# Kernel optimization log

Measured on AMD Instinct MI355X. Metric: run time of the kernel, lower is better.

## Reference

```python
import jax, jax.numpy as jnp
from jax import lax
import numpy as np

K = 3  # kernel_size

def _hamming2d():
    return jnp.asarray(np.outer(np.hamming(K), np.hamming(K)), dtype=jnp.float32)

def setup_inputs() -> dict:
    key = jax.random.key(0)
    k1, k2, k3 = jax.random.split(key, 3)
    B, C, H, W = 4, 256, 256, 256
    comp = 64
    x = jax.random.normal(k1, (B, C, H, W), dtype=jnp.float32)
    # xavier_normal for 1x1 compressor: std = sqrt(2/(fan_in+fan_out))
    w_comp = jax.random.normal(k2, (comp, C), dtype=jnp.float32) * np.sqrt(2.0 / (C + comp))
    # kernel generator: normal std=0.001, zero bias (as in _init_weights)
    w_gen = jax.random.normal(k3, (K * K, comp, 3, 3), dtype=jnp.float32) * 0.001
    b_gen = jnp.zeros((K * K,), dtype=jnp.float32)
    return {"x": x, "w_comp": w_comp, "w_gen": w_gen, "b_gen": b_gen}

def reference(x, w_comp, w_gen, b_gen):
    B, C, H, W = x.shape
    KK = K * K
    # 1x1 channel compression (no bias)
    compressed = jnp.einsum('bchw,oc->bohw', x, w_comp)
    # 3x3 conv, padding=1, with bias -> raw kernel logits (B, KK, H, W)
    logits = lax.conv_general_dilated(
        compressed, w_gen, window_strides=(1, 1), padding='SAME',
        dimension_numbers=('NCHW', 'OIHW', 'NCHW')) + b_gen[None, :, None, None]
    # softmax over the KK kernel taps per spatial position
    kw = jax.nn.softmax(logits, axis=1)
    # NOTE: original uses .view (memory reinterpret), not permute: (B,KK,H,W) -> (B,H,W,K,K)
    kw = kw.reshape(B, H, W, K, K) * _hamming2d()
    kw = kw / (kw.sum(axis=(-1, -2), keepdims=True) + 1e-8)
    kw = jnp.transpose(kw, (0, 3, 4, 1, 2)).reshape(B, KK, H, W)
    # adaptive aggregation: reflect pad + per-tap weighted sum (avoids KK x blowup)
    pad = K // 2
    xp = jnp.pad(x, ((0, 0), (0, 0), (pad, pad), (pad, pad)), mode='reflect')
    agg = jnp.zeros_like(x)
    for i in range(K):
        for j in range(K):
            agg = agg + xp[:, :, i:i + H, j:j + W] * kw[:, i * K + j][:, None]
    highpass = x - agg
    return x + highpass  # use_residual=True
```

## Files before the change

### kernel.cpp

```cpp
#include <hip/hip_runtime.h>
#include <stdint.h>

#define Bd 4
#define Cd 256
#define Hd 256
#define Wd 256
#define HW 65536
#define CM 64
#define KK 9
#define CG 32


typedef __attribute__((ext_vector_type(8))) short bf16x8;
typedef __attribute__((ext_vector_type(4))) float f32x4;

__device__ __forceinline__ uint32_t f2bf1(float f) {
    uint32_t u = __float_as_uint(f);
    return (u + 0x7FFFu + ((u >> 16) & 1u)) >> 16;
}
__device__ __forceinline__ uint32_t pkbf(float lo, float hi) {
    return f2bf1(lo) | (f2bf1(hi) << 16);
}
__device__ __forceinline__ float bf2f(uint32_t u) {
    return __uint_as_float(u << 16);
}

union BF8 { uint32_t u[4]; bf16x8 v; };

__device__ __forceinline__ void loadB(const float* __restrict__ px, int ks,
                                      float4 (&buf)[8]) {
#pragma unroll
    for (int j = 0; j < 8; ++j)
        buf[j] = *(const float4*)(px + (size_t)(ks * 32 + j) * HW);
}

__device__ __forceinline__ void stepMFMA(const float4 (&buf)[8],
                                         const short (*ws)[256], int ks,
                                         int l15, int lhi, int l7,
                                         f32x4 (&acc)[4][4]) {
    BF8 bn[4];
    bn[0].u[0] = pkbf(buf[0].x, buf[1].x);
    bn[0].u[1] = pkbf(buf[2].x, buf[3].x);
    bn[0].u[2] = pkbf(buf[4].x, buf[5].x);
    bn[0].u[3] = pkbf(buf[6].x, buf[7].x);
    bn[1].u[0] = pkbf(buf[0].y, buf[1].y);
    bn[1].u[1] = pkbf(buf[2].y, buf[3].y);
    bn[1].u[2] = pkbf(buf[4].y, buf[5].y);
    bn[1].u[3] = pkbf(buf[6].y, buf[7].y);
    bn[2].u[0] = pkbf(buf[0].z, buf[1].z);
    bn[2].u[1] = pkbf(buf[2].z, buf[3].z);
    bn[2].u[2] = pkbf(buf[4].z, buf[5].z);
    bn[2].u[3] = pkbf(buf[6].z, buf[7].z);
    bn[3].u[0] = pkbf(buf[0].w, buf[1].w);
    bn[3].u[1] = pkbf(buf[2].w, buf[3].w);
    bn[3].u[2] = pkbf(buf[4].w, buf[5].w);
    bn[3].u[3] = pkbf(buf[6].w, buf[7].w);
#pragma unroll
    for (int m = 0; m < 4; ++m) {
        int gg = ((ks << 2) + lhi) ^ l7;
        bf16x8 af = *(const bf16x8*)&ws[m * 16 + l15][gg << 3];
        acc[m][0] = __builtin_amdgcn_mfma_f32_16x16x32_bf16(af, bn[0].v, acc[m][0], 0, 0, 0);
        acc[m][1] = __builtin_amdgcn_mfma_f32_16x16x32_bf16(af, bn[1].v, acc[m][1], 0, 0, 0);
        acc[m][2] = __builtin_amdgcn_mfma_f32_16x16x32_bf16(af, bn[2].v, acc[m][2], 0, 0, 0);
        acc[m][3] = __builtin_amdgcn_mfma_f32_16x16x32_bf16(af, bn[3].v, acc[m][3], 0, 0, 0);
    }
}

__global__ __launch_bounds__(256, 2) void compress_kernel(
    const float* __restrict__ x, const float* __restrict__ w_comp,
    unsigned short* __restrict__ comp)
{
    __shared__ short ws[CM][256];

    int tid = threadIdx.x;
    {
        int o  = tid >> 2;
        int k0 = (tid & 3) << 6;
        const float* wr = w_comp + o * Cd + k0;
        int xr = o & 7;
#pragma unroll
        for (int gi = 0; gi < 8; ++gi) {
            float4 a = *(const float4*)(wr + gi * 8);
            float4 c = *(const float4*)(wr + gi * 8 + 4);
            BF8 g;
            g.u[0] = pkbf(a.x, a.y); g.u[1] = pkbf(a.z, a.w);
            g.u[2] = pkbf(c.x, c.y); g.u[3] = pkbf(c.z, c.w);
            int gg = ((k0 >> 3) + gi) ^ xr;
            *(bf16x8*)&ws[o][gg << 3] = g.v;
        }
    }
    __syncthreads();

    int lane = tid & 63;
    int wv   = tid >> 6;
    int blk  = blockIdx.x;
    int b    = blk >> 8;
    int s0   = ((blk & 255) << 8) + (wv << 6);
    int l15  = lane & 15, lhi = lane >> 4, l7 = lane & 7;

    const float* px = x + (size_t)b * Cd * HW + (size_t)(lhi * 8) * HW + s0 + 4 * l15;

    f32x4 acc[4][4];
    f32x4 zz = {0.f, 0.f, 0.f, 0.f};
#pragma unroll
    for (int m = 0; m < 4; ++m)
#pragma unroll
        for (int n = 0; n < 4; ++n) acc[m][n] = zz;

    float4 pa[8], pb[8];
    loadB(px, 0, pa);
    for (int ks = 0; ks < 8; ks += 2) {
        loadB(px, ks + 1, pb);
        stepMFMA(pa, ws, ks, l15, lhi, l7, acc);
        if (ks + 2 < 8) loadB(px, ks + 2, pa);
        stepMFMA(pb, ws, ks + 1, l15, lhi, l7, acc);
    }

    unsigned short* ob = comp + (size_t)b * CM * HW + s0 + 4 * l15;
#pragma unroll
    for (int m = 0; m < 4; ++m)
#pragma unroll
        for (int r = 0; r < 4; ++r) {
            uint2 pk;
            pk.x = pkbf(acc[m][0][r], acc[m][1][r]);
            pk.y = pkbf(acc[m][2][r], acc[m][3][r]);
            *(uint2*)&ob[(size_t)(m * 16 + lhi * 4 + r) * HW] = pk;
        }
}

__global__ __launch_bounds__(512, 2) void kwgen_kernel(
    const unsigned short* __restrict__ comp, const float* __restrict__ w_gen,
    const float* __restrict__ b_gen, float* __restrict__ kw)
{
    __shared__ float wlds[CM][KK][12];
    for (int i = threadIdx.x; i < KK * CM * 9; i += 512) {
        int t = i / (CM * 9);
        int r = i - t * (CM * 9);
        int c = r / 9;
        int p = r - c * 9;
        wlds[c][t][p] = w_gen[i];
    }
    __syncthreads();

    int lane = threadIdx.x & 63;
    int wid  = threadIdx.x >> 6;
    int half = wid & 1;
    int blk  = blockIdx.x;
    int b    = blk >> 6;
    int h    = ((blk & 63) << 2) + (wid >> 1);
    int w0   = (half << 7) + (lane << 1);
    bool hmv = h > 0, hpv = h < Hd - 1;

    float accv[KK][2];
#pragma unroll
    for (int t = 0; t < KK; ++t) { float bg = b_gen[t]; accv[t][0] = bg; accv[t][1] = bg; }

    const unsigned short* cb = comp + (size_t)b * CM * HW + h * Wd;
    for (int c = 0; c < CM; ++c) {
        const unsigned short* row = cb + (size_t)c * HW;
        const unsigned short* rm  = row - Wd;
        const unsigned short* rp  = row + Wd;
        uint32_t amu = hmv ? *(const uint32_t*)(rm + w0) : 0u;
        uint32_t acu = *(const uint32_t*)(row + w0);
        uint32_t apu = hpv ? *(const uint32_t*)(rp + w0) : 0u;
        float amx = bf2f(amu), amy = bf2f(amu >> 16);
        float acx = bf2f(acu), acy = bf2f(acu >> 16);
        float apx = bf2f(apu), apy = bf2f(apu >> 16);
        float Lm = __shfl_up(amy, 1), Lc = __shfl_up(acy, 1), Lp = __shfl_up(apy, 1);
        float Rm = __shfl_down(amx, 1), Rc = __shfl_down(acx, 1), Rp = __shfl_down(apx, 1);
        if (lane == 0) {
            if (w0 == 0) { Lm = 0.f; Lc = 0.f; Lp = 0.f; }
            else {
                Lm = hmv ? bf2f(rm[w0 - 1]) : 0.f;
                Lc = bf2f(row[w0 - 1]);
                Lp = hpv ? bf2f(rp[w0 - 1]) : 0.f;
            }
        }
        if (lane == 63) {
            int wr = w0 + 2;
            if (wr == Wd) { Rm = 0.f; Rc = 0.f; Rp = 0.f; }
            else {
                Rm = hmv ? bf2f(rm[wr]) : 0.f;
                Rc = bf2f(row[wr]);
                Rp = hpv ? bf2f(rp[wr]) : 0.f;
            }
        }
        float em[4] = {Lm, amx, amy, Rm};
        float ec[4] = {Lc, acx, acy, Rc};
        float ep[4] = {Lp, apx, apy, Rp};
#pragma unroll
        for (int t = 0; t < KK; ++t) {
            const float* wt = &wlds[c][t][0];
#pragma unroll
            for (int j = 0; j < 2; ++j) {
                float a = accv[t][j];
                a = fmaf(em[j],     wt[0], a);
                a = fmaf(em[j + 1], wt[1], a);
                a = fmaf(em[j + 2], wt[2], a);
                a = fmaf(ec[j],     wt[3], a);
                a = fmaf(ec[j + 1], wt[4], a);
                a = fmaf(ec[j + 2], wt[5], a);
                a = fmaf(ep[j],     wt[6], a);
                a = fmaf(ep[j + 1], wt[7], a);
                a = fmaf(ep[j + 2], wt[8], a);
                accv[t][j] = a;
            }
        }
    }
    float inv[2];
#pragma unroll
    for (int j = 0; j < 2; ++j) {
        float m = accv[0][j];
#pragma unroll
        for (int t = 1; t < KK; ++t) m = fmaxf(m, accv[t][j]);
        float sum = 0.f;
#pragma unroll
        for (int t = 0; t < KK; ++t) { accv[t][j] = __expf(accv[t][j] - m); sum += accv[t][j]; }
        inv[j] = 1.f / sum;
    }
    float* ob = kw + (size_t)b * KK * HW + h * Wd + w0;
#pragma unroll
    for (int t = 0; t < KK; ++t) {
        float2 v = make_float2(accv[t][0] * inv[0], accv[t][1] * inv[1]);
        *(float2*)(ob + (size_t)t * HW) = v;
    }
}

__global__ __launch_bounds__(256) void agg_kernel(
    const float* __restrict__ x, const float* __restrict__ kw,
    float* __restrict__ out)
{
    const float HAM[9] = {0.0064f, 0.08f, 0.0064f,
                          0.08f,   1.0f,  0.08f,
                          0.0064f, 0.08f, 0.0064f};
    int lane = threadIdx.x & 63;
    int wid  = threadIdx.x >> 6;
    int blk  = blockIdx.x;
    int h4 = blk & 63;
    int cg = (blk >> 6) & 7;
    int b  = blk >> 9;
    int h  = h4 * 4 + wid;
    int hm = (h == 0) ? 1 : h - 1;
    int hp = (h == Hd - 1) ? Hd - 2 : h + 1;

    float wv[4][9];
    {
        const float4* kv = (const float4*)(kw + (size_t)b * KK * HW
                                              + (size_t)h * (Wd * 9) + lane * 36);
        float t[36];
#pragma unroll
        for (int i = 0; i < 9; ++i) {
            float4 v = kv[i];
            t[i * 4 + 0] = v.x; t[i * 4 + 1] = v.y;
            t[i * 4 + 2] = v.z; t[i * 4 + 3] = v.w;
        }
#pragma unroll
        for (int j = 0; j < 4; ++j) {
            float s = 1e-8f;
#pragma unroll
            for (int p = 0; p < 9; ++p) { float u = t[j * 9 + p] * HAM[p]; wv[j][p] = u; s += u; }
            float inv = 1.f / s;
#pragma unroll
            for (int p = 0; p < 9; ++p) wv[j][p] *= inv;
        }
    }

    const float* xb = x + (size_t)b * Cd * HW;
    float* ob = out + (size_t)b * Cd * HW;
    int c0 = cg * CG;
    for (int c = c0; c < c0 + CG; ++c) {
        const float* xc0 = xb + (size_t)c * HW;
        float4 am = ((const float4*)(xc0 + hm * Wd))[lane];
        float4 ac = ((const float4*)(xc0 + h  * Wd))[lane];
        float4 ap = ((const float4*)(xc0 + hp * Wd))[lane];
        float Lm = __shfl_up(am.w, 1), Lc = __shfl_up(ac.w, 1), Lp = __shfl_up(ap.w, 1);
        float Rm = __shfl_down(am.x, 1), Rc = __shfl_down(ac.x, 1), Rp = __shfl_down(ap.x, 1);
        if (lane == 0)  { Lm = am.y; Lc = ac.y; Lp = ap.y; }
        if (lane == 63) { Rm = am.z; Rc = ac.z; Rp = ap.z; }
        float em[6] = {Lm, am.x, am.y, am.z, am.w, Rm};
        float ec[6] = {Lc, ac.x, ac.y, ac.z, ac.w, Rc};
        float ep[6] = {Lp, ap.x, ap.y, ap.z, ap.w, Rp};
        float o4[4];
#pragma unroll
        for (int j = 0; j < 4; ++j) {
            float agg = em[j] * wv[j][0];
            agg = fmaf(em[j + 1], wv[j][1], agg);
            agg = fmaf(em[j + 2], wv[j][2], agg);
            agg = fmaf(ec[j],     wv[j][3], agg);
            agg = fmaf(ec[j + 1], wv[j][4], agg);
            agg = fmaf(ec[j + 2], wv[j][5], agg);
            agg = fmaf(ep[j],     wv[j][6], agg);
            agg = fmaf(ep[j + 1], wv[j][7], agg);
            agg = fmaf(ep[j + 2], wv[j][8], agg);
            o4[j] = 2.f * ec[j + 1] - agg;
        }
        float4 o = {o4[0], o4[1], o4[2], o4[3]};
        ((float4*)(ob + (size_t)c * HW + h * Wd))[lane] = o;
    }
}

extern "C" void kernel_launch(void* const* d_in, const int* in_sizes, int n_in,
                              void* d_out, int out_size, void* d_ws, size_t ws_size,
                              hipStream_t stream) {
    const float* x      = (const float*)d_in[0];
    const float* w_comp = (const float*)d_in[1];
    const float* w_gen  = (const float*)d_in[2];
    const float* b_gen  = (const float*)d_in[3];
    float* out  = (float*)d_out;
    unsigned short* comp = (unsigned short*)d_ws;
    float* kw = (float*)((char*)d_ws + (size_t)Bd * CM * HW * sizeof(unsigned short));

    compress_kernel<<<1024, 256, 0, stream>>>(x, w_comp, comp);
    kwgen_kernel<<<256, 512, 0, stream>>>(comp, w_gen, b_gen, kw);
    agg_kernel<<<2048, 256, 0, stream>>>(x, kw, out);
}
```

Measured before the change: 263.4 us.

## Stage compress-kernel x tiles through LDS via async global_load_lds double buffering

The compress kernel now loads each 32-channel slice of x with direct global-to-LDS loads into a per-wave double buffer, replacing register-staged float4 prefetches. Each step waits on vmcnt and reads its slice from LDS while the next slice's load is in flight. The aim is to cut VGPR pressure and keep more memory traffic outstanding. It adds about 64KB of LDS per block and drops the occupancy hint from 2 to 1 blocks per SM, and it relies on hand-written waitcnt ordering.

```diff
diff --git a/kernel.cpp b/kernel.cpp
--- a/kernel.cpp
+++ b/kernel.cpp
@@ -26,13 +26,6 @@
 }
 
 union BF8 { uint32_t u[4]; bf16x8 v; };
-
-__device__ __forceinline__ void loadB(const float* __restrict__ px, int ks,
-                                      float4 (&buf)[8]) {
-#pragma unroll
-    for (int j = 0; j < 8; ++j)
-        buf[j] = *(const float4*)(px + (size_t)(ks * 32 + j) * HW);
-}
 
 __device__ __forceinline__ void stepMFMA(const float4 (&buf)[8],
                                          const short (*ws)[256], int ks,
@@ -66,11 +59,12 @@
     }
 }
 
-__global__ __launch_bounds__(256, 2) void compress_kernel(
+__global__ __launch_bounds__(256, 1) void compress_kernel(
     const float* __restrict__ x, const float* __restrict__ w_comp,
     unsigned short* __restrict__ comp)
 {
     __shared__ short ws[CM][256];
+    __shared__ float xstg[4][2][2048];
 
     int tid = threadIdx.x;
     {
@@ -98,7 +92,20 @@
     int s0   = ((blk & 255) << 8) + (wv << 6);
     int l15  = lane & 15, lhi = lane >> 4, l7 = lane & 7;
 
-    const float* px = x + (size_t)b * Cd * HW + (size_t)(lhi * 8) * HW + s0 + 4 * l15;
+    const float* xg = x + (size_t)b * Cd * HW + s0 + l15 * 4;
+    float* stg0 = &xstg[wv][0][0];
+    float* stg1 = &xstg[wv][1][0];
+
+#pragma unroll
+    for (int j = 0; j < 8; ++j)
+        __builtin_amdgcn_global_load_lds(
+            (const uint32_t*)(xg + (size_t)(j * 4 + lhi) * HW),
+            (uint32_t*)(stg0 + j * 256), 16, 0, 0);
+#pragma unroll
+    for (int j = 0; j < 8; ++j)
+        __builtin_amdgcn_global_load_lds(
+            (const uint32_t*)(xg + (size_t)(32 + j * 4 + lhi) * HW),
+            (uint32_t*)(stg1 + j * 256), 16, 0, 0);
 
     f32x4 acc[4][4];
     f32x4 zz = {0.f, 0.f, 0.f, 0.f};
@@ -107,13 +114,28 @@
 #pragma unroll
         for (int n = 0; n < 4; ++n) acc[m][n] = zz;
 
-    float4 pa[8], pb[8];
-    loadB(px, 0, pa);
-    for (int ks = 0; ks < 8; ks += 2) {
-        loadB(px, ks + 1, pb);
+#pragma unroll
+    for (int ks = 0; ks < 8; ++ks) {
+        float* stg = (ks & 1) ? stg1 : stg0;
+        if (ks < 7) { asm volatile("s_waitcnt vmcnt(8)" ::: "memory"); }
+        else        { asm volatile("s_waitcnt vmcnt(0)" ::: "memory"); }
+        __builtin_amdgcn_sched_barrier(0);
+        float4 pa[8];
+#pragma unroll
+        for (int jj = 0; jj < 8; ++jj) {
+            int rr = lhi * 8 + jj;
+            pa[jj] = *(const float4*)(stg + (rr >> 2) * 256 + ((rr & 3) * 16 + l15) * 4);
+        }
+        asm volatile("s_waitcnt lgkmcnt(0)" ::: "memory");
+        __builtin_amdgcn_sched_barrier(0);
+        if (ks + 2 < 8) {
+#pragma unroll
+            for (int j = 0; j < 8; ++j)
+                __builtin_amdgcn_global_load_lds(
+                    (const uint32_t*)(xg + (size_t)((ks + 2) * 32 + j * 4 + lhi) * HW),
+                    (uint32_t*)(stg + j * 256), 16, 0, 0);
+        }
         stepMFMA(pa, ws, ks, l15, lhi, l7, acc);
-        if (ks + 2 < 8) loadB(px, ks + 2, pa);
-        stepMFMA(pb, ws, ks + 1, l15, lhi, l7, acc);
     }
 
     unsigned short* ob = comp + (size_t)b * CM * HW + s0 + 4 * l15;
```

After: 269.0 us. 1.02x slower.
